# Optimization experiments

Measured on AMD Instinct MI355X. Metric: run time of the kernel, lower is better.

## Reference

```python
import jax, jax.numpy as jnp
import numpy as np

D_MODEL = 1024
N_HEADS = 16
D_HEAD = D_MODEL // N_HEADS
BSZ, SEQ = 1, 4096


def setup_inputs() -> dict:
    key = jax.random.key(0)
    ks = jax.random.split(key, 7)
    scale = 1.0 / np.sqrt(D_MODEL)
    q = jax.random.normal(ks[0], (BSZ, SEQ, D_MODEL), dtype=jnp.float32)
    k = jax.random.normal(ks[1], (BSZ, SEQ, D_MODEL), dtype=jnp.float32)
    v = jax.random.normal(ks[2], (BSZ, SEQ, D_MODEL), dtype=jnp.float32)
    Wq = jax.random.normal(ks[3], (D_MODEL, D_MODEL), dtype=jnp.float32) * scale
    Wk = jax.random.normal(ks[4], (D_MODEL, D_MODEL), dtype=jnp.float32) * scale
    Wv = jax.random.normal(ks[5], (D_MODEL, D_MODEL), dtype=jnp.float32) * scale
    Wo = jax.random.normal(ks[6], (D_MODEL, D_MODEL), dtype=jnp.float32) * scale
    # causal mask: 1 = attend, 0 = masked (matches torch masked_fill(mask == 0, -inf))
    mask = jnp.tril(jnp.ones((SEQ, SEQ), dtype=jnp.int32))[None, None, :, :]
    return {"q": q, "k": k, "v": v, "mask": mask, "Wq": Wq, "Wk": Wk, "Wv": Wv, "Wo": Wo}


def reference(q, k, v, mask, Wq, Wk, Wv, Wo):
    bsz, seq, _ = q.shape
    # nn.Linear(d,d,bias=False): y = x @ W.T
    Q = (q @ Wq.T).reshape(bsz, seq, N_HEADS, D_HEAD).transpose(0, 2, 1, 3)
    K = (k @ Wk.T).reshape(bsz, seq, N_HEADS, D_HEAD).transpose(0, 2, 1, 3)
    V = (v @ Wv.T).reshape(bsz, seq, N_HEADS, D_HEAD).transpose(0, 2, 1, 3)
    scores = jnp.einsum("bhqd,bhkd->bhqk", Q, K) / np.sqrt(D_HEAD).astype(np.float32)
    scores = jnp.where(mask == 0, -jnp.inf, scores)
    attn = jax.nn.softmax(scores, axis=-1)
    out = jnp.einsum("bhqk,bhkd->bhqd", attn, V)
    out = out.transpose(0, 2, 1, 3).reshape(bsz, seq, D_MODEL)
    return out @ Wo.T
```

## Files before the change

kernel.cpp:

```cpp
#include <hip/hip_runtime.h>


typedef __attribute__((ext_vector_type(8))) short bf16x8;
typedef __attribute__((ext_vector_type(4))) float f32x4;
typedef __attribute__((ext_vector_type(16))) float f32x16;

#define S_LEN 4096
#define DM 1024
#define NH 16
#define DH 64

static __device__ __forceinline__ unsigned short f2bf(float f) {
  union { float f; unsigned u; } x; x.f = f;
  unsigned u = x.u;
  u += 0x7fffu + ((u >> 16) & 1u);
  return (unsigned short)(u >> 16);
}

static __device__ __forceinline__ unsigned pk2(float lo, float hi) {
  unsigned r;
  asm("v_cvt_pk_bf16_f32 %0, %1, %2" : "=v"(r) : "v"(lo), "v"(hi));
  return r;
}

static __device__ __forceinline__ void swap32u(unsigned& a, unsigned& b) {
  asm("v_permlane32_swap_b32 %0, %1" : "+v"(a), "+v"(b));
}

static __device__ __forceinline__ float exp2_(float x) {
#if __has_builtin(__builtin_amdgcn_exp2f)
  return __builtin_amdgcn_exp2f(x);
#else
  return exp2f(x);
#endif
}

#define GLL16(gsrc, ldst)                                                      \
  __builtin_amdgcn_global_load_lds(                                            \
      (const __attribute__((address_space(1))) void*)(gsrc),                   \
      (__attribute__((address_space(3))) void*)(ldst), 16, 0, 0)

struct CastArgs {
  const float* src[8];
  unsigned short* dst[8];
  int n[8];
  float scl[8];
};

__global__ __launch_bounds__(256) void cast_all(CastArgs a) {
  int which = blockIdx.y;
  const float* __restrict__ src = a.src[which];
  unsigned short* __restrict__ dst = a.dst[which];
  int n = a.n[which];
  float s = a.scl[which];
  int i = (blockIdx.x * 256 + threadIdx.x) * 8;
  if (i >= n) return;
  f32x4 v0 = *(const f32x4*)(src + i);
  f32x4 v1 = *(const f32x4*)(src + i + 4);
  union { bf16x8 v; unsigned short u[8]; } o;
#pragma unroll
  for (int j = 0; j < 4; j++) { o.u[j] = f2bf(v0[j] * s); o.u[4 + j] = f2bf(v1[j] * s); }
  *(bf16x8*)(dst + i) = o.v;
}

static __device__ __forceinline__ void gemm_body(
    const unsigned short* __restrict__ A, const unsigned short* __restrict__ B,
    void* __restrict__ Cout, int mode, unsigned short* As, unsigned short* Bs) {
  const int K = 1024;
  int tid = threadIdx.x;
  int wid = tid >> 6, lane = tid & 63;
  int m0 = blockIdx.y * 128, n0 = blockIdx.x * 128;
  int wr = (wid >> 1) * 64, wc = (wid & 1) * 64;
  int g = lane >> 4, r = lane & 15;

  const int srow = wid * 8 + (lane >> 3);
  const int scol = 8 * ((lane & 7) ^ ((lane >> 3) & 7));
  const unsigned short* gA[4];
  const unsigned short* gB[4];
#pragma unroll
  for (int rr = 0; rr < 4; rr++) {
    gA[rr] = A + (size_t)(m0 + rr * 32 + srow) * K + scol;
    gB[rr] = B + (size_t)(n0 + rr * 32 + srow) * K + scol;
  }

  f32x4 acc[4][4] = {};
  const int rsw = (r & 7) << 3;

  for (int k0 = 0; k0 < K; k0 += 64) {
#pragma unroll
    for (int rr = 0; rr < 4; rr++) {
      GLL16(gA[rr] + k0, As + wid * 512 + rr * 2048);
      GLL16(gB[rr] + k0, Bs + wid * 512 + rr * 2048);
    }
    __syncthreads();

#pragma unroll
    for (int kk = 0; kk < 64; kk += 32) {
      bf16x8 af[4], bfr[4];
#pragma unroll
      for (int mi = 0; mi < 4; mi++)
        af[mi] = *(const bf16x8*)&As[(wr + mi * 16 + r) * 64 + ((kk + g * 8) ^ rsw)];
#pragma unroll
      for (int ni = 0; ni < 4; ni++)
        bfr[ni] = *(const bf16x8*)&Bs[(wc + ni * 16 + r) * 64 + ((kk + g * 8) ^ rsw)];
#pragma unroll
      for (int mi = 0; mi < 4; mi++)
#pragma unroll
        for (int ni = 0; ni < 4; ni++)
          acc[mi][ni] = __builtin_amdgcn_mfma_f32_16x16x32_bf16(
              af[mi], bfr[ni], acc[mi][ni], 0, 0, 0);
    }
    __syncthreads();
  }

  if (mode == 0) {
    float* C = (float*)Cout;
#pragma unroll
    for (int mi = 0; mi < 4; mi++) {
      int row = m0 + wr + mi * 16 + g * 4;
#pragma unroll
      for (int ni = 0; ni < 4; ni++) {
        int c = n0 + wc + ni * 16 + r;
#pragma unroll
        for (int j = 0; j < 4; j++)
          C[(size_t)(row + j) * DM + c] = acc[mi][ni][j];
      }
    }
  } else if (mode == 1) {
    unsigned short* Cb = (unsigned short*)Cout;
#pragma unroll
    for (int mi = 0; mi < 4; mi++) {
      int row = m0 + wr + mi * 16 + g * 4;
#pragma unroll
      for (int ni = 0; ni < 4; ni++) {
        int c = n0 + wc + ni * 16 + r;
        int h = c >> 6, d = c & 63;
#pragma unroll
        for (int j = 0; j < 4; j++)
          Cb[(size_t)h * (S_LEN * DH) + (size_t)(row + j) * DH + d] =
              f2bf(acc[mi][ni][j]);
      }
    }
  } else {
    unsigned short* Cb = (unsigned short*)Cout;
#pragma unroll
    for (int mi = 0; mi < 4; mi++) {
      int row = m0 + wr + mi * 16 + g * 4;
#pragma unroll
      for (int ni = 0; ni < 4; ni++) {
        int c = n0 + wc + ni * 16 + r;
        int h = c >> 6, d = c & 63;
#pragma unroll
        for (int j = 0; j < 4; j++) {
          int s = row + j;
          Cb[(size_t)h * (S_LEN * DH) + (size_t)(s >> 6) * 4096 + d * 64 + (s & 63)] =
              f2bf(acc[mi][ni][j]);
        }
      }
    }
  }
}

struct ProjArgs {
  const unsigned short* A[3];
  const unsigned short* B[3];
  unsigned short* C[3];
  int mode[3];
};

__global__ __launch_bounds__(256, 2) void gemm_proj(ProjArgs p) {
  __shared__ unsigned short As[8192];
  __shared__ unsigned short Bs[8192];
  int z = blockIdx.z;
  gemm_body(p.A[z], p.B[z], p.C[z], p.mode[z], As, Bs);
}

__global__ __launch_bounds__(256, 2) void gemm_one(
    const unsigned short* __restrict__ A, const unsigned short* __restrict__ B,
    void* __restrict__ Cout, int mode) {
  __shared__ unsigned short As[8192];
  __shared__ unsigned short Bs[8192];
  gemm_body(A, B, Cout, mode, As, Bs);
}

__global__ __launch_bounds__(512, 4) void attn_fwd(
    const unsigned short* __restrict__ Qh, const unsigned short* __restrict__ Kh,
    const unsigned short* __restrict__ V4, unsigned short* __restrict__ O) {
  __shared__ char smem[65536];

  const int b = blockIdx.x;
  const int hd = b & 15;
  const int t = b >> 4;
  const int qe = (t < 16) ? (31 - 2 * t) : (2 * (t - 16));
  const int q0 = qe * 128;
  const int nt = qe + 1;

  const int tid = threadIdx.x;
  const int gg = tid >> 8;
  const int ww = (tid >> 6) & 3;
  const int lane = tid & 63;
  const int l31 = lane & 31, hi = lane >> 5;
  const int qi = ww;
  const int qw = q0 + qi * 32;
  const int qrow = qw + l31;
  const int sw = (l31 & 7) << 4;

  const unsigned short* Qb = Qh + (size_t)hd * (S_LEN * DH);
  const char* Kb = (const char*)(Kh + (size_t)hd * (S_LEN * DH));
  const char* Vb = (const char*)(V4 + (size_t)hd * (S_LEN * DH));

  bf16x8 qf[4];
#pragma unroll
  for (int m = 0; m < 4; m++)
    qf[m] = *(const bf16x8*)&Qb[(size_t)qrow * DH + m * 16 + hi * 8];

  const int roleV = (ww >= 2);
  const int wv = ww & 1;
  const char* gb = roleV ? Vb : Kb;
  int soff[4];
#pragma unroll
  for (int q2 = 0; q2 < 4; q2++) {
    int rowl = wv * 32 + q2 * 8 + (lane >> 3);
    int cb = ((lane & 7) * 16) ^ (((lane >> 3) & 7) << 4);
    soff[q2] = rowl * 128 + cb;
  }
  const int ldsc = gg * 32768 + roleV * 8192 + wv * 4096;

  f32x16 oacc[2] = {};
  float m_r = 16.0f, l_r = 0.f;

  {
    const char* gp = gb + (long)(gg * nt) * 8192;
#pragma unroll
    for (int q2 = 0; q2 < 4; q2++)
      GLL16(gp + soff[q2], smem + ldsc + q2 * 1024);
  }
  __syncthreads();

  int db = 0;
  for (int it = 0; it < nt; ++it) {
    if (it + 1 < nt) {
      const char* gp = gb + (long)(gg * nt + it + 1) * 8192;
      char* lb = smem + ldsc + (db ^ 1) * 16384;
#pragma unroll
      for (int q2 = 0; q2 < 4; q2++)
        GLL16(gp + soff[q2], lb + q2 * 1024);
    }
    const int kv0 = (gg * nt + it) * 64;
    const char* Kc = smem + gg * 32768 + db * 16384;
    const char* Vc = Kc + 8192;

    if (kv0 <= qw + 31) {
      const bool hiP = (kv0 + 32 <= qw + 31);
      const bool interior = (kv0 + 63 <= qw);
      f32x16 s0 = {}, s1 = {};
#pragma unroll
      for (int m = 0; m < 4; m++) {
        bf16x8 kf = *(const bf16x8*)(Kc + l31 * 128 + ((m * 32 + hi * 16) ^ sw));
        s0 = __builtin_amdgcn_mfma_f32_32x32x16_bf16(kf, qf[m], s0, 0, 0, 0);
      }
      if (hiP) {
#pragma unroll
        for (int m = 0; m < 4; m++) {
          bf16x8 kf = *(const bf16x8*)(Kc + (32 + l31) * 128 + ((m * 32 + hi * 16) ^ sw));
          s1 = __builtin_amdgcn_mfma_f32_32x32x16_bf16(kf, qf[m], s1, 0, 0, 0);
        }
      }
      bf16x8 vf0[4];
#pragma unroll
      for (int i = 0; i < 4; i++) {
        const int dt = i >> 1, n = i & 1;
        vf0[i] = *(const bf16x8*)(Vc + (dt * 32 + l31) * 128 +
                   ((n * 32 + hi * 16) ^ sw));
      }
      if (!interior) {
#pragma unroll
        for (int rg = 0; rg < 16; rg++) {
          const int kvl = (rg & 3) + 8 * (rg >> 2) + 4 * hi;
          s0[rg] = (kv0 + kvl <= qrow) ? s0[rg] : -1e30f;
          s1[rg] = (hiP && kv0 + 32 + kvl <= qrow) ? s1[rg] : -1e30f;
        }
      }
#pragma unroll
      for (int rg = 0; rg < 16; rg++) {
        s0[rg] = exp2_(s0[rg] - m_r);
        s1[rg] = exp2_(s1[rg] - m_r);
      }
      float t0 = fmaxf(fmaxf(s0[0], s0[1]), s0[2]);
      float t1 = fmaxf(fmaxf(s0[3], s0[4]), s0[5]);
      float t2 = fmaxf(fmaxf(s0[6], s0[7]), s0[8]);
      float t3 = fmaxf(fmaxf(s0[9], s0[10]), s0[11]);
      float t4 = fmaxf(fmaxf(s0[12], s0[13]), s0[14]);
      float t5 = fmaxf(fmaxf(s0[15], s1[0]), s1[1]);
      float t6 = fmaxf(fmaxf(s1[2], s1[3]), s1[4]);
      float t7 = fmaxf(fmaxf(s1[5], s1[6]), s1[7]);
      float t8 = fmaxf(fmaxf(s1[8], s1[9]), s1[10]);
      float t9 = fmaxf(fmaxf(s1[11], s1[12]), s1[13]);
      float ta = fmaxf(s1[14], s1[15]);
      float u0 = fmaxf(fmaxf(t0, t1), t2);
      float u1 = fmaxf(fmaxf(t3, t4), t5);
      float u2 = fmaxf(fmaxf(t6, t7), t8);
      float u3 = fmaxf(t9, ta);
      float mxp = fmaxf(fmaxf(u0, u1), fmaxf(u2, u3));
      if (__any(mxp > 1024.0f)) {
        float mrow = fmaxf(mxp, __shfl_xor(mxp, 32, 64));
        float sc = 1.0f / mrow;
        m_r += __log2f(mrow);
        l_r *= sc;
#pragma unroll
        for (int rg = 0; rg < 16; rg++) { s0[rg] *= sc; s1[rg] *= sc; }
#pragma unroll
        for (int dt = 0; dt < 2; dt++)
#pragma unroll
          for (int rg = 0; rg < 16; rg++) oacc[dt][rg] *= sc;
      }
      float r0 = (s0[0] + s0[1]) + (s0[2] + s0[3]);
      float r1 = (s0[4] + s0[5]) + (s0[6] + s0[7]);
      float r2 = (s0[8] + s0[9]) + (s0[10] + s0[11]);
      float r3 = (s0[12] + s0[13]) + (s0[14] + s0[15]);
      float r4 = (s1[0] + s1[1]) + (s1[2] + s1[3]);
      float r5 = (s1[4] + s1[5]) + (s1[6] + s1[7]);
      float r6 = (s1[8] + s1[9]) + (s1[10] + s1[11]);
      float r7 = (s1[12] + s1[13]) + (s1[14] + s1[15]);
      l_r += ((r0 + r1) + (r2 + r3)) + ((r4 + r5) + (r6 + r7));
#pragma unroll
      for (int c = 0; c < 2; c++) {
        if (c == 0 || hiP) {
          const f32x16 P = c ? s1 : s0;
#pragma unroll
          for (int n = 0; n < 2; n++) {
            unsigned a0 = pk2(P[8 * n + 0], P[8 * n + 1]);
            unsigned a1 = pk2(P[8 * n + 2], P[8 * n + 3]);
            unsigned b0 = pk2(P[8 * n + 4], P[8 * n + 5]);
            unsigned b1 = pk2(P[8 * n + 6], P[8 * n + 7]);
            swap32u(a0, b0);
            swap32u(a1, b1);
            union { unsigned w[4]; bf16x8 v; } u;
            u.w[0] = a0; u.w[1] = a1; u.w[2] = b0; u.w[3] = b1;
#pragma unroll
            for (int dt = 0; dt < 2; dt++) {
              bf16x8 vf = (c == 0) ? vf0[dt * 2 + n]
                        : *(const bf16x8*)(Vc + (dt * 32 + l31) * 128 +
                             ((64 + n * 32 + hi * 16) ^ sw));
              oacc[dt] = __builtin_amdgcn_mfma_f32_32x32x16_bf16(
                  vf, u.v, oacc[dt], 0, 0, 0);
            }
          }
        }
      }
    }
    __syncthreads();
    db ^= 1;
  }

  l_r += __shfl_xor(l_r, 32, 64);

  float* scr = (float*)smem;
  const int sbase = (qi * 64 + lane) * 35;
  if (gg == 1) {
#pragma unroll
    for (int dt = 0; dt < 2; dt++)
#pragma unroll
      for (int rg = 0; rg < 16; rg++) scr[sbase + dt * 16 + rg] = oacc[dt][rg];
    scr[sbase + 32] = m_r;
    scr[sbase + 33] = l_r;
  }
  __syncthreads();
  if (gg == 0) {
    float mB = scr[sbase + 32], lB = scr[sbase + 33];
    float mS = fmaxf(m_r, mB);
    float sA = exp2_(m_r - mS);
    float sB = exp2_(mB - mS);
    float rl = 1.0f / (l_r * sA + lB * sB);
    float fA = sA * rl, fB = sB * rl;
#pragma unroll
    for (int dt = 0; dt < 2; dt++)
#pragma unroll
      for (int blk = 0; blk < 4; blk++) {
        float v0 = oacc[dt][blk * 4 + 0] * fA + scr[sbase + dt * 16 + blk * 4 + 0] * fB;
        float v1 = oacc[dt][blk * 4 + 1] * fA + scr[sbase + dt * 16 + blk * 4 + 1] * fB;
        float v2 = oacc[dt][blk * 4 + 2] * fA + scr[sbase + dt * 16 + blk * 4 + 2] * fB;
        float v3 = oacc[dt][blk * 4 + 3] * fA + scr[sbase + dt * 16 + blk * 4 + 3] * fB;
        uint2 st; st.x = pk2(v0, v1); st.y = pk2(v2, v3);
        int d0 = dt * 32 + blk * 8 + 4 * hi;
        *(uint2*)&O[(size_t)qrow * DM + hd * DH + d0] = st;
      }
  }
}

extern "C" void kernel_launch(void* const* d_in, const int* in_sizes, int n_in,
                              void* d_out, int out_size, void* d_ws, size_t ws_size,
                              hipStream_t stream) {
  const float* q = (const float*)d_in[0];
  const float* k = (const float*)d_in[1];
  const float* v = (const float*)d_in[2];
  const float* Wq = (const float*)d_in[4];
  const float* Wk = (const float*)d_in[5];
  const float* Wv = (const float*)d_in[6];
  const float* Wo = (const float*)d_in[7];

  unsigned short* W = (unsigned short*)d_ws;
  const int SM = S_LEN * DM;
  const int WM = DM * DM;
  unsigned short* qb  = W;
  unsigned short* kb  = qb + SM;
  unsigned short* vb  = kb + SM;
  unsigned short* Wqb = vb + SM;
  unsigned short* Wkb = Wqb + WM;
  unsigned short* Wvb = Wkb + WM;
  unsigned short* Wob = Wvb + WM;
  unsigned short* Qh  = Wob + WM;
  unsigned short* Kh  = Qh + SM;
  unsigned short* V4  = Kh + SM;
  unsigned short* Ob  = V4 + SM;

  CastArgs ca;
  ca.src[0] = q;  ca.dst[0] = qb;  ca.n[0] = SM; ca.scl[0] = 1.f;
  ca.src[1] = k;  ca.dst[1] = kb;  ca.n[1] = SM; ca.scl[1] = 1.f;
  ca.src[2] = v;  ca.dst[2] = vb;  ca.n[2] = SM; ca.scl[2] = 1.f;
  ca.src[3] = Wq; ca.dst[3] = Wqb; ca.n[3] = WM; ca.scl[3] = 0.125f * 1.44269504f;
  ca.src[4] = Wk; ca.dst[4] = Wkb; ca.n[4] = WM; ca.scl[4] = 1.f;
  ca.src[5] = Wv; ca.dst[5] = Wvb; ca.n[5] = WM; ca.scl[5] = 1.f;
  ca.src[6] = Wo; ca.dst[6] = Wob; ca.n[6] = WM; ca.scl[6] = 1.f;
  ca.src[7] = Wo; ca.dst[7] = Wob; ca.n[7] = 0;  ca.scl[7] = 1.f;
  cast_all<<<dim3(2048, 8), 256, 0, stream>>>(ca);

  ProjArgs pa;
  pa.A[0] = qb; pa.B[0] = Wqb; pa.C[0] = Qh; pa.mode[0] = 1;
  pa.A[1] = kb; pa.B[1] = Wkb; pa.C[1] = Kh; pa.mode[1] = 1;
  pa.A[2] = vb; pa.B[2] = Wvb; pa.C[2] = V4; pa.mode[2] = 2;
  gemm_proj<<<dim3(8, 32, 3), 256, 0, stream>>>(pa);

  attn_fwd<<<dim3(512), 512, 0, stream>>>(Qh, Kh, V4, Ob);

  gemm_one<<<dim3(8, 32), 256, 0, stream>>>(Ob, Wob, d_out, 0);
}
```

Before: 125.6 us.

## Shrink attention blocks to 64 query rows with 32-key tiles and 1024 blocks

The attention kernel now uses 256-thread blocks covering 64 query rows instead of 512-thread blocks covering 128. The KV tile shrinks from 64 to 32 keys, so each wave computes one score fragment instead of two. Two warps split K and V loading, with a new V swizzle for the 64-byte-row layout. The rescale check now tests the row sum instead of the row max. The aim is better load balance and occupancy across the causal triangle, in exchange for more loop iterations and syncs and less K/V reuse per block.

```diff
diff --git a/kernel.cpp b/kernel.cpp
--- a/kernel.cpp
+++ b/kernel.cpp
@@ -183,27 +183,29 @@
   gemm_body(A, B, Cout, mode, As, Bs);
 }
 
-__global__ __launch_bounds__(512, 4) void attn_fwd(
+__global__ __launch_bounds__(256, 4) void attn_fwd(
     const unsigned short* __restrict__ Qh, const unsigned short* __restrict__ Kh,
     const unsigned short* __restrict__ V4, unsigned short* __restrict__ O) {
-  __shared__ char smem[65536];
+  __shared__ char smem[32768];
 
   const int b = blockIdx.x;
   const int hd = b & 15;
-  const int t = b >> 4;
-  const int qe = (t < 16) ? (31 - 2 * t) : (2 * (t - 16));
-  const int q0 = qe * 128;
-  const int nt = qe + 1;
+  const int u = b >> 4;
+  const int g4 = u & 15, j4 = u >> 4;
+  const int e = (j4 == 0) ? g4 : (j4 == 1) ? (31 - g4)
+              : (j4 == 2) ? (32 + g4) : (63 - g4);
+  const int q0 = e * 64;
+  const int nt = e + 1;
 
   const int tid = threadIdx.x;
-  const int gg = tid >> 8;
-  const int ww = (tid >> 6) & 3;
+  const int ww = tid >> 6;
+  const int gg = ww >> 1, qi = ww & 1;
   const int lane = tid & 63;
   const int l31 = lane & 31, hi = lane >> 5;
-  const int qi = ww;
   const int qw = q0 + qi * 32;
   const int qrow = qw + l31;
-  const int sw = (l31 & 7) << 4;
+  const int sw8 = (l31 & 7) << 4;
+  const int swv = (((l31 & 3) ^ ((l31 >> 2) & 3))) << 4;
 
   const unsigned short* Qb = Qh + (size_t)hd * (S_LEN * DH);
   const char* Kb = (const char*)(Kh + (size_t)hd * (S_LEN * DH));
@@ -214,23 +216,27 @@
   for (int m = 0; m < 4; m++)
     qf[m] = *(const bf16x8*)&Qb[(size_t)qrow * DH + m * 16 + hi * 8];
 
-  const int roleV = (ww >= 2);
-  const int wv = ww & 1;
-  const char* gb = roleV ? Vb : Kb;
   int soff[4];
 #pragma unroll
   for (int q2 = 0; q2 < 4; q2++) {
-    int rowl = wv * 32 + q2 * 8 + (lane >> 3);
-    int cb = ((lane & 7) * 16) ^ (((lane >> 3) & 7) << 4);
-    soff[q2] = rowl * 128 + cb;
-  }
-  const int ldsc = gg * 32768 + roleV * 8192 + wv * 4096;
+    if (qi == 0) {
+      int row = q2 * 8 + (lane >> 3);
+      soff[q2] = row * 128 + (((lane & 7) * 16) ^ (((lane >> 3) & 7) << 4));
+    } else {
+      int row = q2 * 16 + (lane >> 2);
+      soff[q2] = row * 128 +
+                 (((lane & 3) * 16) ^ ((((lane >> 2) & 3) ^ ((lane >> 4) & 3)) << 4));
+    }
+  }
+  const int ldsc = gg * 16384 + qi * 4096;
 
   f32x16 oacc[2] = {};
   float m_r = 16.0f, l_r = 0.f;
 
   {
-    const char* gp = gb + (long)(gg * nt) * 8192;
+    const int T = gg * nt;
+    const char* gp = (qi == 0) ? (Kb + (size_t)T * 4096)
+                               : (Vb + (size_t)(T >> 1) * 8192 + (T & 1) * 64);
 #pragma unroll
     for (int q2 = 0; q2 < 4; q2++)
       GLL16(gp + soff[q2], smem + ldsc + q2 * 1024);
@@ -240,112 +246,70 @@
   int db = 0;
   for (int it = 0; it < nt; ++it) {
     if (it + 1 < nt) {
-      const char* gp = gb + (long)(gg * nt + it + 1) * 8192;
-      char* lb = smem + ldsc + (db ^ 1) * 16384;
+      const int T = gg * nt + it + 1;
+      const char* gp = (qi == 0) ? (Kb + (size_t)T * 4096)
+                                 : (Vb + (size_t)(T >> 1) * 8192 + (T & 1) * 64);
+      char* lb = smem + gg * 16384 + (db ^ 1) * 8192 + qi * 4096;
 #pragma unroll
       for (int q2 = 0; q2 < 4; q2++)
         GLL16(gp + soff[q2], lb + q2 * 1024);
     }
-    const int kv0 = (gg * nt + it) * 64;
-    const char* Kc = smem + gg * 32768 + db * 16384;
-    const char* Vc = Kc + 8192;
+    const int kv0 = (gg * nt + it) * 32;
+    const char* Kc = smem + gg * 16384 + db * 8192;
+    const char* Vc = Kc + 4096;
 
     if (kv0 <= qw + 31) {
-      const bool hiP = (kv0 + 32 <= qw + 31);
-      const bool interior = (kv0 + 63 <= qw);
-      f32x16 s0 = {}, s1 = {};
+      const bool interior = (kv0 + 31 <= qw);
+      f32x16 s0 = {};
 #pragma unroll
       for (int m = 0; m < 4; m++) {
-        bf16x8 kf = *(const bf16x8*)(Kc + l31 * 128 + ((m * 32 + hi * 16) ^ sw));
+        bf16x8 kf = *(const bf16x8*)(Kc + l31 * 128 + ((m * 32 + hi * 16) ^ sw8));
         s0 = __builtin_amdgcn_mfma_f32_32x32x16_bf16(kf, qf[m], s0, 0, 0, 0);
-      }
-      if (hiP) {
-#pragma unroll
-        for (int m = 0; m < 4; m++) {
-          bf16x8 kf = *(const bf16x8*)(Kc + (32 + l31) * 128 + ((m * 32 + hi * 16) ^ sw));
-          s1 = __builtin_amdgcn_mfma_f32_32x32x16_bf16(kf, qf[m], s1, 0, 0, 0);
-        }
-      }
-      bf16x8 vf0[4];
-#pragma unroll
-      for (int i = 0; i < 4; i++) {
-        const int dt = i >> 1, n = i & 1;
-        vf0[i] = *(const bf16x8*)(Vc + (dt * 32 + l31) * 128 +
-                   ((n * 32 + hi * 16) ^ sw));
       }
       if (!interior) {
 #pragma unroll
         for (int rg = 0; rg < 16; rg++) {
           const int kvl = (rg & 3) + 8 * (rg >> 2) + 4 * hi;
           s0[rg] = (kv0 + kvl <= qrow) ? s0[rg] : -1e30f;
-          s1[rg] = (hiP && kv0 + 32 + kvl <= qrow) ? s1[rg] : -1e30f;
         }
       }
 #pragma unroll
-      for (int rg = 0; rg < 16; rg++) {
-        s0[rg] = exp2_(s0[rg] - m_r);
-        s1[rg] = exp2_(s1[rg] - m_r);
-      }
-      float t0 = fmaxf(fmaxf(s0[0], s0[1]), s0[2]);
-      float t1 = fmaxf(fmaxf(s0[3], s0[4]), s0[5]);
-      float t2 = fmaxf(fmaxf(s0[6], s0[7]), s0[8]);
-      float t3 = fmaxf(fmaxf(s0[9], s0[10]), s0[11]);
-      float t4 = fmaxf(fmaxf(s0[12], s0[13]), s0[14]);
-      float t5 = fmaxf(fmaxf(s0[15], s1[0]), s1[1]);
-      float t6 = fmaxf(fmaxf(s1[2], s1[3]), s1[4]);
-      float t7 = fmaxf(fmaxf(s1[5], s1[6]), s1[7]);
-      float t8 = fmaxf(fmaxf(s1[8], s1[9]), s1[10]);
-      float t9 = fmaxf(fmaxf(s1[11], s1[12]), s1[13]);
-      float ta = fmaxf(s1[14], s1[15]);
-      float u0 = fmaxf(fmaxf(t0, t1), t2);
-      float u1 = fmaxf(fmaxf(t3, t4), t5);
-      float u2 = fmaxf(fmaxf(t6, t7), t8);
-      float u3 = fmaxf(t9, ta);
-      float mxp = fmaxf(fmaxf(u0, u1), fmaxf(u2, u3));
-      if (__any(mxp > 1024.0f)) {
-        float mrow = fmaxf(mxp, __shfl_xor(mxp, 32, 64));
-        float sc = 1.0f / mrow;
-        m_r += __log2f(mrow);
-        l_r *= sc;
-#pragma unroll
-        for (int rg = 0; rg < 16; rg++) { s0[rg] *= sc; s1[rg] *= sc; }
-#pragma unroll
-        for (int dt = 0; dt < 2; dt++)
-#pragma unroll
-          for (int rg = 0; rg < 16; rg++) oacc[dt][rg] *= sc;
-      }
+      for (int rg = 0; rg < 16; rg++) s0[rg] = exp2_(s0[rg] - m_r);
       float r0 = (s0[0] + s0[1]) + (s0[2] + s0[3]);
       float r1 = (s0[4] + s0[5]) + (s0[6] + s0[7]);
       float r2 = (s0[8] + s0[9]) + (s0[10] + s0[11]);
       float r3 = (s0[12] + s0[13]) + (s0[14] + s0[15]);
-      float r4 = (s1[0] + s1[1]) + (s1[2] + s1[3]);
-      float r5 = (s1[4] + s1[5]) + (s1[6] + s1[7]);
-      float r6 = (s1[8] + s1[9]) + (s1[10] + s1[11]);
-      float r7 = (s1[12] + s1[13]) + (s1[14] + s1[15]);
-      l_r += ((r0 + r1) + (r2 + r3)) + ((r4 + r5) + (r6 + r7));
-#pragma unroll
-      for (int c = 0; c < 2; c++) {
-        if (c == 0 || hiP) {
-          const f32x16 P = c ? s1 : s0;
-#pragma unroll
-          for (int n = 0; n < 2; n++) {
-            unsigned a0 = pk2(P[8 * n + 0], P[8 * n + 1]);
-            unsigned a1 = pk2(P[8 * n + 2], P[8 * n + 3]);
-            unsigned b0 = pk2(P[8 * n + 4], P[8 * n + 5]);
-            unsigned b1 = pk2(P[8 * n + 6], P[8 * n + 7]);
-            swap32u(a0, b0);
-            swap32u(a1, b1);
-            union { unsigned w[4]; bf16x8 v; } u;
-            u.w[0] = a0; u.w[1] = a1; u.w[2] = b0; u.w[3] = b1;
-#pragma unroll
-            for (int dt = 0; dt < 2; dt++) {
-              bf16x8 vf = (c == 0) ? vf0[dt * 2 + n]
-                        : *(const bf16x8*)(Vc + (dt * 32 + l31) * 128 +
-                             ((64 + n * 32 + hi * 16) ^ sw));
-              oacc[dt] = __builtin_amdgcn_mfma_f32_32x32x16_bf16(
-                  vf, u.v, oacc[dt], 0, 0, 0);
-            }
-          }
+      float rs = (r0 + r1) + (r2 + r3);
+      if (__any(rs > 1e30f)) {
+        float rsx = rs + __shfl_xor(rs, 32, 64);
+        float sc = 1.0f / rsx;
+        m_r += __log2f(rsx);
+        l_r *= sc;
+#pragma unroll
+        for (int rg = 0; rg < 16; rg++) s0[rg] *= sc;
+#pragma unroll
+        for (int dt = 0; dt < 2; dt++)
+#pragma unroll
+          for (int rg = 0; rg < 16; rg++) oacc[dt][rg] *= sc;
+        rs *= sc;
+      }
+      l_r += rs;
+#pragma unroll
+      for (int n = 0; n < 2; n++) {
+        unsigned a0 = pk2(s0[8 * n + 0], s0[8 * n + 1]);
+        unsigned a1 = pk2(s0[8 * n + 2], s0[8 * n + 3]);
+        unsigned b0 = pk2(s0[8 * n + 4], s0[8 * n + 5]);
+        unsigned b1 = pk2(s0[8 * n + 6], s0[8 * n + 7]);
+        swap32u(a0, b0);
+        swap32u(a1, b1);
+        union { unsigned w[4]; bf16x8 v; } fr;
+        fr.w[0] = a0; fr.w[1] = a1; fr.w[2] = b0; fr.w[3] = b1;
+#pragma unroll
+        for (int dt = 0; dt < 2; dt++) {
+          bf16x8 vf = *(const bf16x8*)(Vc + (dt * 32 + l31) * 64 +
+                        ((n * 32 + hi * 16) ^ swv));
+          oacc[dt] = __builtin_amdgcn_mfma_f32_32x32x16_bf16(
+              vf, fr.v, oacc[dt], 0, 0, 0);
         }
       }
     }
@@ -431,7 +395,7 @@
   pa.A[2] = vb; pa.B[2] = Wvb; pa.C[2] = V4; pa.mode[2] = 2;
   gemm_proj<<<dim3(8, 32, 3), 256, 0, stream>>>(pa);
 
-  attn_fwd<<<dim3(512), 512, 0, stream>>>(Qh, Kh, V4, Ob);
+  attn_fwd<<<dim3(1024), 256, 0, stream>>>(Qh, Kh, V4, Ob);
 
   gemm_one<<<dim3(8, 32), 256, 0, stream>>>(Ob, Wob, d_out, 0);
 }
```

New measurement: 133.9 us. +6.6%, slower.

## Drop intra-block KV split in attention and use cheaper sum-based rescale check

Applied to the files above, without the earlier changes.

The attention kernel stops splitting each query block's KV range across two 256-thread groups. Each 256-thread block now walks all of its causal KV tiles itself, and blocks are ordered heaviest first. This removes the shared-memory merge and the extra barrier, and halves LDS use. It also replaces the per-tile max reduction and its threshold check with a check on the row-sum overflowing, which removes many fmax instructions per tile. The cost is a longer serial loop per block and fewer waves per query block, and the overflow test is looser, which relies on score magnitudes staying bounded.

```diff
diff --git a/kernel.cpp b/kernel.cpp
--- a/kernel.cpp
+++ b/kernel.cpp
@@ -183,25 +183,22 @@
   gemm_body(A, B, Cout, mode, As, Bs);
 }
 
-__global__ __launch_bounds__(512, 4) void attn_fwd(
+__global__ __launch_bounds__(256, 4) void attn_fwd(
     const unsigned short* __restrict__ Qh, const unsigned short* __restrict__ Kh,
     const unsigned short* __restrict__ V4, unsigned short* __restrict__ O) {
-  __shared__ char smem[65536];
+  __shared__ char smem[32768];
 
   const int b = blockIdx.x;
   const int hd = b & 15;
-  const int t = b >> 4;
-  const int qe = (t < 16) ? (31 - 2 * t) : (2 * (t - 16));
-  const int q0 = qe * 128;
-  const int nt = qe + 1;
+  const int e = 31 - (b >> 4);
+  const int q0 = e * 128;
+  const int nt = 2 * e + 2;
 
   const int tid = threadIdx.x;
-  const int gg = tid >> 8;
-  const int ww = (tid >> 6) & 3;
+  const int ww = tid >> 6;
   const int lane = tid & 63;
   const int l31 = lane & 31, hi = lane >> 5;
-  const int qi = ww;
-  const int qw = q0 + qi * 32;
+  const int qw = q0 + ww * 32;
   const int qrow = qw + l31;
   const int sw = (l31 & 7) << 4;
 
@@ -224,30 +221,27 @@
     int cb = ((lane & 7) * 16) ^ (((lane >> 3) & 7) << 4);
     soff[q2] = rowl * 128 + cb;
   }
-  const int ldsc = gg * 32768 + roleV * 8192 + wv * 4096;
+  const int ldsc = roleV * 8192 + wv * 4096;
 
   f32x16 oacc[2] = {};
   float m_r = 16.0f, l_r = 0.f;
 
-  {
-    const char* gp = gb + (long)(gg * nt) * 8192;
-#pragma unroll
-    for (int q2 = 0; q2 < 4; q2++)
-      GLL16(gp + soff[q2], smem + ldsc + q2 * 1024);
-  }
+#pragma unroll
+  for (int q2 = 0; q2 < 4; q2++)
+    GLL16(gb + soff[q2], smem + ldsc + q2 * 1024);
   __syncthreads();
 
   int db = 0;
   for (int it = 0; it < nt; ++it) {
     if (it + 1 < nt) {
-      const char* gp = gb + (long)(gg * nt + it + 1) * 8192;
-      char* lb = smem + ldsc + (db ^ 1) * 16384;
+      const char* gp = gb + (size_t)(it + 1) * 8192;
+      char* lb = smem + (db ^ 1) * 16384 + ldsc;
 #pragma unroll
       for (int q2 = 0; q2 < 4; q2++)
         GLL16(gp + soff[q2], lb + q2 * 1024);
     }
-    const int kv0 = (gg * nt + it) * 64;
-    const char* Kc = smem + gg * 32768 + db * 16384;
+    const int kv0 = it * 64;
+    const char* Kc = smem + db * 16384;
     const char* Vc = Kc + 8192;
 
     if (kv0 <= qw + 31) {
@@ -285,34 +279,6 @@
       for (int rg = 0; rg < 16; rg++) {
         s0[rg] = exp2_(s0[rg] - m_r);
         s1[rg] = exp2_(s1[rg] - m_r);
-      }
-      float t0 = fmaxf(fmaxf(s0[0], s0[1]), s0[2]);
-      float t1 = fmaxf(fmaxf(s0[3], s0[4]), s0[5]);
-      float t2 = fmaxf(fmaxf(s0[6], s0[7]), s0[8]);
-      float t3 = fmaxf(fmaxf(s0[9], s0[10]), s0[11]);
-      float t4 = fmaxf(fmaxf(s0[12], s0[13]), s0[14]);
-      float t5 = fmaxf(fmaxf(s0[15], s1[0]), s1[1]);
-      float t6 = fmaxf(fmaxf(s1[2], s1[3]), s1[4]);
-      float t7 = fmaxf(fmaxf(s1[5], s1[6]), s1[7]);
-      float t8 = fmaxf(fmaxf(s1[8], s1[9]), s1[10]);
-      float t9 = fmaxf(fmaxf(s1[11], s1[12]), s1[13]);
-      float ta = fmaxf(s1[14], s1[15]);
-      float u0 = fmaxf(fmaxf(t0, t1), t2);
-      float u1 = fmaxf(fmaxf(t3, t4), t5);
-      float u2 = fmaxf(fmaxf(t6, t7), t8);
-      float u3 = fmaxf(t9, ta);
-      float mxp = fmaxf(fmaxf(u0, u1), fmaxf(u2, u3));
-      if (__any(mxp > 1024.0f)) {
-        float mrow = fmaxf(mxp, __shfl_xor(mxp, 32, 64));
-        float sc = 1.0f / mrow;
-        m_r += __log2f(mrow);
-        l_r *= sc;
-#pragma unroll
-        for (int rg = 0; rg < 16; rg++) { s0[rg] *= sc; s1[rg] *= sc; }
-#pragma unroll
-        for (int dt = 0; dt < 2; dt++)
-#pragma unroll
-          for (int rg = 0; rg < 16; rg++) oacc[dt][rg] *= sc;
       }
       float r0 = (s0[0] + s0[1]) + (s0[2] + s0[3]);
       float r1 = (s0[4] + s0[5]) + (s0[6] + s0[7]);
@@ -322,7 +288,21 @@
       float r5 = (s1[4] + s1[5]) + (s1[6] + s1[7]);
       float r6 = (s1[8] + s1[9]) + (s1[10] + s1[11]);
       float r7 = (s1[12] + s1[13]) + (s1[14] + s1[15]);
-      l_r += ((r0 + r1) + (r2 + r3)) + ((r4 + r5) + (r6 + r7));
+      float rs = ((r0 + r1) + (r2 + r3)) + ((r4 + r5) + (r6 + r7));
+      if (__any(rs > 1e30f)) {
+        float rsx = rs + __shfl_xor(rs, 32, 64);
+        float sc = 1.0f / rsx;
+        m_r += __log2f(rsx);
+        l_r *= sc;
+#pragma unroll
+        for (int rg = 0; rg < 16; rg++) { s0[rg] *= sc; s1[rg] *= sc; }
+#pragma unroll
+        for (int dt = 0; dt < 2; dt++)
+#pragma unroll
+          for (int rg = 0; rg < 16; rg++) oacc[dt][rg] *= sc;
+        rs *= sc;
+      }
+      l_r += rs;
 #pragma unroll
       for (int c = 0; c < 2; c++) {
         if (c == 0 || hiP) {
@@ -354,38 +334,17 @@
   }
 
   l_r += __shfl_xor(l_r, 32, 64);
-
-  float* scr = (float*)smem;
-  const int sbase = (qi * 64 + lane) * 35;
-  if (gg == 1) {
-#pragma unroll
-    for (int dt = 0; dt < 2; dt++)
-#pragma unroll
-      for (int rg = 0; rg < 16; rg++) scr[sbase + dt * 16 + rg] = oacc[dt][rg];
-    scr[sbase + 32] = m_r;
-    scr[sbase + 33] = l_r;
-  }
-  __syncthreads();
-  if (gg == 0) {
-    float mB = scr[sbase + 32], lB = scr[sbase + 33];
-    float mS = fmaxf(m_r, mB);
-    float sA = exp2_(m_r - mS);
-    float sB = exp2_(mB - mS);
-    float rl = 1.0f / (l_r * sA + lB * sB);
-    float fA = sA * rl, fB = sB * rl;
-#pragma unroll
-    for (int dt = 0; dt < 2; dt++)
-#pragma unroll
-      for (int blk = 0; blk < 4; blk++) {
-        float v0 = oacc[dt][blk * 4 + 0] * fA + scr[sbase + dt * 16 + blk * 4 + 0] * fB;
-        float v1 = oacc[dt][blk * 4 + 1] * fA + scr[sbase + dt * 16 + blk * 4 + 1] * fB;
-        float v2 = oacc[dt][blk * 4 + 2] * fA + scr[sbase + dt * 16 + blk * 4 + 2] * fB;
-        float v3 = oacc[dt][blk * 4 + 3] * fA + scr[sbase + dt * 16 + blk * 4 + 3] * fB;
-        uint2 st; st.x = pk2(v0, v1); st.y = pk2(v2, v3);
-        int d0 = dt * 32 + blk * 8 + 4 * hi;
-        *(uint2*)&O[(size_t)qrow * DM + hd * DH + d0] = st;
-      }
-  }
+  float rl = 1.0f / l_r;
+#pragma unroll
+  for (int dt = 0; dt < 2; dt++)
+#pragma unroll
+    for (int blk = 0; blk < 4; blk++) {
+      unsigned w0 = pk2(oacc[dt][blk * 4 + 0] * rl, oacc[dt][blk * 4 + 1] * rl);
+      unsigned w1 = pk2(oacc[dt][blk * 4 + 2] * rl, oacc[dt][blk * 4 + 3] * rl);
+      uint2 st; st.x = w0; st.y = w1;
+      int d0 = dt * 32 + blk * 8 + 4 * hi;
+      *(uint2*)&O[(size_t)qrow * DM + hd * DH + d0] = st;
+    }
 }
 
 extern "C" void kernel_launch(void* const* d_in, const int* in_sizes, int n_in,
@@ -431,7 +390,7 @@
   pa.A[2] = vb; pa.B[2] = Wvb; pa.C[2] = V4; pa.mode[2] = 2;
   gemm_proj<<<dim3(8, 32, 3), 256, 0, stream>>>(pa);
 
-  attn_fwd<<<dim3(512), 512, 0, stream>>>(Qh, Kh, V4, Ob);
+  attn_fwd<<<dim3(512), 256, 0, stream>>>(Qh, Kh, V4, Ob);
 
   gemm_one<<<dim3(8, 32), 256, 0, stream>>>(Ob, Wob, d_out, 0);
 }
```

New measurement: 204.3 us. 1.63x slower.
